# Kernel optimization log

Measured on AMD Instinct MI355X. Metric: run time of the kernel, lower is better.

Reference implementation:

```python
import jax, jax.numpy as jnp
import numpy as np

L_MAX = 119
D_MODEL = 128
N_HEADS = 4
HEAD_DIM = 32


def _rope_tables():
    # matches torch: inv_freq over arange(0,128,2)/128, t=arange(119), cast to bf16
    channel_range = jnp.arange(0, D_MODEL, 2, dtype=jnp.float32)
    inv_freq = 1.0 / (10000.0 ** (channel_range / D_MODEL))
    t = jnp.arange(L_MAX, dtype=jnp.float32)
    freqs = jnp.outer(t, inv_freq)  # (119, 64)
    return jnp.cos(freqs).astype(jnp.bfloat16), jnp.sin(freqs).astype(jnp.bfloat16)


def _apply_rotary(x, cos, sin):
    # x: (b, l, 128); half-rotation on the full model dim (pre head-split)
    l = x.shape[1]
    d = x.shape[-1] // 2
    x1, x2 = x[..., :d], x[..., d:]
    c, s = cos[:l], sin[:l]
    y1 = x1 * c + x2 * s
    y2 = x1 * (-s) + x2 * c
    return jnp.concatenate([y1, y2], axis=-1).astype(x.dtype)


def setup_inputs() -> dict:
    key = jax.random.key(0)
    k1, k2, k3, k4, k5 = jax.random.split(key, 5)
    b, l = 2048, L_MAX
    return {
        "x": jax.random.normal(k1, (b, l, D_MODEL), dtype=jnp.float32),
        "W_qkv": jax.random.normal(k2, (3 * D_MODEL, D_MODEL), dtype=jnp.float32) * 0.05,
        "b_qkv": jax.random.normal(k3, (3 * D_MODEL,), dtype=jnp.float32) * 0.02,
        "W_fc2": jax.random.normal(k4, (D_MODEL, D_MODEL), dtype=jnp.float32) * 0.05,
        "b_fc2": jax.random.normal(k5, (D_MODEL,), dtype=jnp.float32) * 0.02,
    }


def reference(x, W_qkv, b_qkv, W_fc2, b_fc2):
    b, l, _ = x.shape
    cos, sin = _rope_tables()

    qkv = x @ W_qkv.T + b_qkv  # (b, l, 384)
    q, k, v = jnp.split(qkv, 3, axis=-1)
    q = _apply_rotary(q, cos, sin)
    k = _apply_rotary(k, cos, sin)

    # faithful to source: view(b, l, 32, 4) then 'b l d h -> b h l d'
    def split_heads(t):
        return t.reshape(b, l, HEAD_DIM, N_HEADS).transpose(0, 3, 1, 2)  # (b, h, l, d)

    q, k, v = split_heads(q), split_heads(k), split_heads(v)

    scale = 1.0 / np.sqrt(HEAD_DIM)
    scores = jnp.einsum("bhld,bhmd->bhlm", q, k) * scale  # (b, h, l, l)
    causal = jnp.tril(jnp.ones((l, l), dtype=bool))
    scores = jnp.where(causal, scores, jnp.float32(-jnp.inf))
    attn = jax.nn.softmax(scores, axis=-1)
    y = jnp.einsum("bhlm,bhmd->bhld", attn, v)  # (b, h, l, d)

    # faithful to source: transpose(1,2) then view(b, l, 128) -> layout h*32+d
    y = y.transpose(0, 2, 1, 3).reshape(b, l, D_MODEL)
    y = y @ W_fc2.T + b_fc2
    return jax.nn.silu(y)
```

## Files before the change

kernel.cpp:

```cpp
#include <hip/hip_runtime.h>
#include <hip/hip_bf16.h>
#include <math.h>


#define L_SEQ 119
#define D_MODEL 128
#define SCALE 0.17677669529663687f
#define NEGINF -1e30f

typedef __bf16 bf16x8 __attribute__((ext_vector_type(8)));
typedef __bf16 bf16x2 __attribute__((ext_vector_type(2)));
typedef float f32x4 __attribute__((ext_vector_type(4)));
typedef float f32x16 __attribute__((ext_vector_type(16)));

__global__ void prep_kernel(const float* __restrict__ Wqkv,
                            const float* __restrict__ bqkv,
                            const float* __restrict__ Wfc2,
                            unsigned* __restrict__ tabu,
                            __bf16* __restrict__ Wb, float* __restrict__ bb2,
                            __bf16* __restrict__ Wf2b) {
  int i = blockIdx.x * 256 + threadIdx.x;
  {
    int j = i & 7, lane = (i >> 3) & 63, ks = (i >> 9) & 7, nt = i >> 12;
    int d = lane & 31;
    int h = nt / 3, qkv = nt % 3;
    int k = ks * 16 + (lane >> 5) * 8 + j;
    Wb[i] = (__bf16)Wqkv[(qkv * 128 + d * 4 + h) * 128 + k];
  }
  if (i < 384) {
    int nt2 = i >> 5, dd = i & 31;
    bb2[i] = bqkv[(nt2 % 3) * 128 + dd * 4 + (nt2 / 3)];
  }
  if (i < 16384) {
    int j = i & 7, lane = (i >> 3) & 63, kb = (i >> 9) & 3, nt = i >> 11;
    int n = nt * 16 + (lane & 15);
    int k = kb * 32 + (lane >> 4) * 8 + j;
    Wf2b[i] = (__bf16)Wfc2[n * 128 + k];
  }
  if (i < L_SEQ * 64) {
    int l = i >> 6, j = i & 63;
    float inv = 1.0f / powf(10000.0f, (float)(2 * j) / 128.0f);
    float f = (float)l * inv;
    union { bf16x2 v; unsigned u; } cs;
    cs.v[0] = (__bf16)cosf(f);
    cs.v[1] = (__bf16)sinf(f);
    tabu[i] = cs.u;
  }
}

__global__ __launch_bounds__(512) void fused_all(
    const float* __restrict__ x, const __bf16* __restrict__ Wb,
    const float* __restrict__ bb2, const unsigned* __restrict__ tabu,
    const __bf16* __restrict__ Wf2b, const float* __restrict__ bfc2,
    float* __restrict__ out) {
  __shared__ __align__(16) __bf16 qs[4 * 128 * 40];
  __shared__ __align__(16) __bf16 ksm[4 * 128 * 40];
  __shared__ __align__(16) __bf16 vT[4 * 32 * 128];
  __shared__ unsigned tabL[L_SEQ * 65];

  const int t = threadIdx.x, b = blockIdx.x;
  const int lane = t & 63, wv = t >> 6;
  const int ln31 = lane & 31, hi = lane >> 5;

  for (int i = t; i < L_SEQ * 64; i += 512)
    tabL[(i >> 6) * 65 + (i & 63)] = tabu[i];
  for (int i = t; i < 4 * 32 * 9; i += 512) {
    int hd = i / 9, cc = L_SEQ + i % 9, d = hd & 31;
    vT[hd * 128 + (cc ^ ((d & 7) << 3))] = (__bf16)0.0f;
  }
  __syncthreads();

  const int mt = wv & 3, g2 = wv >> 2;
  const int l_me = mt * 32 + ln31;
  const bool live = (l_me < L_SEQ);
  {
    int xr = live ? l_me : (L_SEQ - 1);
    const float* xrow = x + ((size_t)b * L_SEQ + xr) * 128;
    bf16x8 af[8];
#pragma unroll
    for (int ks = 0; ks < 8; ++ks) {
      float4 lo = *(const float4*)&xrow[ks * 16 + hi * 8];
      float4 hi4 = *(const float4*)&xrow[ks * 16 + hi * 8 + 4];
      bf16x8 v;
      v[0] = (__bf16)lo.x; v[1] = (__bf16)lo.y; v[2] = (__bf16)lo.z; v[3] = (__bf16)lo.w;
      v[4] = (__bf16)hi4.x; v[5] = (__bf16)hi4.y; v[6] = (__bf16)hi4.z; v[7] = (__bf16)hi4.w;
      af[ks] = v;
    }
#pragma unroll
    for (int r = 0; r < 3; ++r) {
      const int nt0 = g2 * 6 + 2 * r, nt1 = nt0 + 1;
      f32x16 a0 = {}, a1 = {};
#pragma unroll
      for (int ks = 0; ks < 8; ++ks) {
        bf16x8 wf0 = *(const bf16x8*)&Wb[(((nt0 * 8 + ks) * 64) + lane) * 8];
        bf16x8 wf1 = *(const bf16x8*)&Wb[(((nt1 * 8 + ks) * 64) + lane) * 8];
        a0 = __builtin_amdgcn_mfma_f32_32x32x16_bf16(wf0, af[ks], a0, 0, 0, 0);
        a1 = __builtin_amdgcn_mfma_f32_32x32x16_bf16(wf1, af[ks], a1, 0, 0, 0);
      }
#pragma unroll
      for (int e = 0; e < 2; ++e) {
        const int nt = e ? nt1 : nt0;
        const f32x16& A = e ? a1 : a0;
        const int h = nt / 3, qkv = nt % 3;
        if (qkv < 2) {
          __bf16* base = (qkv == 0) ? qs : ksm;
          if (live) {
#pragma unroll
            for (int rg = 0; rg < 8; ++rg) {
              const int c_lo = (rg & 3) + 8 * (rg >> 2);
              int d = c_lo + 4 * hi;
              union { bf16x2 v; unsigned u; } cs;
              cs.u = tabL[l_me * 65 + 4 * d + h];
              float c = (float)cs.v[0], s = (float)cs.v[1];
              float v1 = A[rg] + bb2[nt * 32 + d];
              float v2 = A[rg + 8] + bb2[nt * 32 + d + 16];
              if (qkv == 0) { v1 *= SCALE; v2 *= SCALE; }
              union { bf16x2 v; unsigned u; } pk;
              pk.v[0] = (__bf16)(v1 * c + v2 * s);
              pk.v[1] = (__bf16)(v2 * c - v1 * s);
              *(unsigned*)&base[(h * 128 + l_me) * 40 + 2 * d] = pk.u;
            }
          }
        } else {
          if (live) {
#pragma unroll
            for (int rg = 0; rg < 16; ++rg) {
              const int d = (rg & 3) + 8 * (rg >> 2) + 4 * hi;
              float val = A[rg] + bb2[nt * 32 + d];
              vT[(h * 32 + d) * 128 + (l_me ^ ((d & 7) << 3))] = (__bf16)val;
            }
          }
        }
      }
    }
  }
  __syncthreads();

  {
    const int h = wv >> 1;
#pragma unroll
    for (int ts = 0; ts < 2; ++ts) {
      const int qt = ts ? (3 - (wv & 1)) : (wv & 1);
      bf16x8 qf0 = *(const bf16x8*)&qs[(h * 128 + qt * 32 + ln31) * 40 + hi * 8];
      bf16x8 qf1 = *(const bf16x8*)&qs[(h * 128 + qt * 32 + ln31) * 40 + 16 + hi * 8];
      f32x16 s[4];
#pragma unroll
      for (int kt = 0; kt < 4; ++kt) {
        if (kt <= qt) {
          bf16x8 kf0 = *(const bf16x8*)&ksm[(h * 128 + kt * 32 + ln31) * 40 + hi * 8];
          bf16x8 kf1 = *(const bf16x8*)&ksm[(h * 128 + kt * 32 + ln31) * 40 + 16 + hi * 8];
          f32x16 z = {};
          z = __builtin_amdgcn_mfma_f32_32x32x16_bf16(kf0, qf0, z, 0, 0, 0);
          s[kt] = __builtin_amdgcn_mfma_f32_32x32x16_bf16(kf1, qf1, z, 0, 0, 0);
        }
      }
      {
#pragma unroll
        for (int rg = 0; rg < 16; ++rg) {
          const int c_lo = (rg & 3) + 8 * (rg >> 2);
#pragma unroll
          for (int kt = 0; kt < 4; ++kt) {
            if (kt == qt) {
              int crow = c_lo + 4 * hi;
              s[kt][rg] = (crow <= ln31) ? s[kt][rg] : NEGINF;
            }
          }
        }
      }
      float mx = NEGINF;
#pragma unroll
      for (int kt = 0; kt < 4; ++kt)
        if (kt <= qt)
#pragma unroll
          for (int rg = 0; rg < 16; ++rg) mx = fmaxf(mx, s[kt][rg]);
      mx = fmaxf(mx, __shfl_xor(mx, 32));
      float sum = 0.0f;
#pragma unroll
      for (int kt = 0; kt < 4; ++kt)
        if (kt <= qt)
#pragma unroll
          for (int rg = 0; rg < 16; ++rg) {
            s[kt][rg] = __expf(s[kt][rg] - mx);
            sum += s[kt][rg];
          }
      sum += __shfl_xor(sum, 32);
      float inv = 1.0f / sum;
      unsigned pk[4][8];
#pragma unroll
      for (int kt = 0; kt < 4; ++kt) {
        if (kt <= qt) {
#pragma unroll
          for (int p = 0; p < 8; ++p) {
            union { bf16x2 v; unsigned u; } w;
            w.v[0] = (__bf16)(s[kt][2 * p] * inv);
            w.v[1] = (__bf16)(s[kt][2 * p + 1] * inv);
            pk[kt][p] = w.u;
          }
        }
      }
      f32x16 o = {};
#pragma unroll
      for (int kt = 0; kt < 4; ++kt) {
        if (kt <= qt) {
#pragma unroll
          for (int m = 0; m < 2; ++m) {
            unsigned f0 = (unsigned)__shfl_xor((int)pk[kt][4 * m + 0], 32);
            unsigned f1 = (unsigned)__shfl_xor((int)pk[kt][4 * m + 1], 32);
            unsigned f2 = (unsigned)__shfl_xor((int)pk[kt][4 * m + 2], 32);
            unsigned f3 = (unsigned)__shfl_xor((int)pk[kt][4 * m + 3], 32);
            union { unsigned w[4]; bf16x8 v; } Aw;
            Aw.w[0] = hi ? f2 : pk[kt][4 * m + 0];
            Aw.w[1] = hi ? f3 : pk[kt][4 * m + 1];
            Aw.w[2] = hi ? pk[kt][4 * m + 2] : f0;
            Aw.w[3] = hi ? pk[kt][4 * m + 3] : f1;
            bf16x8 vf = *(const bf16x8*)&vT[(h * 32 + ln31) * 128 +
                ((kt * 32 + m * 16 + hi * 8) ^ ((ln31 & 7) << 3))];
            o = __builtin_amdgcn_mfma_f32_32x32x16_bf16(Aw.v, vf, o, 0, 0, 0);
          }
        }
      }
#pragma unroll
      for (int rg = 0; rg < 16; ++rg) {
        const int c_lo = (rg & 3) + 8 * (rg >> 2);
        int l = qt * 32 + c_lo + 4 * hi;
        if (l < L_SEQ)
          out[((size_t)b * L_SEQ + l) * 128 + h * 32 + ln31] = o[rg];
      }
    }
  }

  __syncthreads();
  {
    const int ln15 = lane & 15, kg = lane >> 4;
    int yr = wv * 16 + ln15;
    if (yr > L_SEQ - 1) yr = L_SEQ - 1;
    const float* yrow = out + ((size_t)b * L_SEQ + yr) * 128;
    bf16x8 af2[4];
#pragma unroll
    for (int kb = 0; kb < 4; ++kb) {
      float4 lo = *(const float4*)&yrow[kb * 32 + kg * 8];
      float4 hi4 = *(const float4*)&yrow[kb * 32 + kg * 8 + 4];
      bf16x8 v;
      v[0] = (__bf16)lo.x; v[1] = (__bf16)lo.y; v[2] = (__bf16)lo.z; v[3] = (__bf16)lo.w;
      v[4] = (__bf16)hi4.x; v[5] = (__bf16)hi4.y; v[6] = (__bf16)hi4.z; v[7] = (__bf16)hi4.w;
      af2[kb] = v;
    }
    float bc[8];
#pragma unroll
    for (int nt = 0; nt < 8; ++nt) bc[nt] = bfc2[nt * 16 + ln15];
    f32x4 acc2[8] = {};
#pragma unroll
    for (int nt = 0; nt < 8; ++nt)
#pragma unroll
      for (int kb = 0; kb < 4; ++kb)
        acc2[nt] = __builtin_amdgcn_mfma_f32_16x16x32_bf16(
            af2[kb], *(const bf16x8*)&Wf2b[(((nt * 4 + kb) * 64) + lane) * 8],
            acc2[nt], 0, 0, 0);
#pragma unroll
    for (int nt = 0; nt < 8; ++nt)
#pragma unroll
      for (int r = 0; r < 4; ++r) {
        int row = wv * 16 + kg * 4 + r, c = nt * 16 + ln15;
        if (row < L_SEQ) {
          float vv = acc2[nt][r] + bc[nt];
          out[((size_t)b * L_SEQ + row) * 128 + c] = vv / (1.0f + __expf(-vv));
        }
      }
  }
}

extern "C" void kernel_launch(void* const* d_in, const int* in_sizes, int n_in,
                              void* d_out, int out_size, void* d_ws,
                              size_t ws_size, hipStream_t stream) {
  const float* x = (const float*)d_in[0];
  const float* Wqkv = (const float*)d_in[1];
  const float* bqkv = (const float*)d_in[2];
  const float* Wfc2 = (const float*)d_in[3];
  const float* bfc2 = (const float*)d_in[4];
  float* out = (float*)d_out;

  char* ws = (char*)d_ws;
  unsigned* tabu = (unsigned*)ws;
  __bf16* Wb = (__bf16*)(ws + 30720);
  float* bb2 = (float*)(ws + 30720 + 98304);
  __bf16* Wf2b = (__bf16*)(ws + 30720 + 98304 + 1536);

  const int B = in_sizes[0] / (L_SEQ * D_MODEL);
  prep_kernel<<<192, 256, 0, stream>>>(Wqkv, bqkv, Wfc2, tabu, Wb, bb2, Wf2b);
  fused_all<<<B, 512, 0, stream>>>(x, Wb, bb2, tabu, Wf2b, bfc2, out);
}
```

Measured before the change: 217.6 us.

## Double block size to 1024 threads and split work across 16 waves

Launches 16 waves per block instead of 8. In the QKV stage each wave now computes one head's q/k/v tiles for one 32-row slab instead of six n-tiles. In attention each wave handles a single query tile instead of two. In FC2 each wave computes half of the output columns. The aim is to shorten each wave's serial chain and raise parallelism within the block, at the cost of higher register pressure under the 1024 launch bound and possible occupancy limits from LDS use per block.

```diff
diff --git a/kernel.cpp b/kernel.cpp
--- a/kernel.cpp
+++ b/kernel.cpp
@@ -48,7 +48,7 @@
   }
 }
 
-__global__ __launch_bounds__(512) void fused_all(
+__global__ __launch_bounds__(1024) void fused_all(
     const float* __restrict__ x, const __bf16* __restrict__ Wb,
     const float* __restrict__ bb2, const unsigned* __restrict__ tabu,
     const __bf16* __restrict__ Wf2b, const float* __restrict__ bfc2,
@@ -62,15 +62,15 @@
   const int lane = t & 63, wv = t >> 6;
   const int ln31 = lane & 31, hi = lane >> 5;
 
-  for (int i = t; i < L_SEQ * 64; i += 512)
+  for (int i = t; i < L_SEQ * 64; i += 1024)
     tabL[(i >> 6) * 65 + (i & 63)] = tabu[i];
-  for (int i = t; i < 4 * 32 * 9; i += 512) {
+  for (int i = t; i < 4 * 32 * 9; i += 1024) {
     int hd = i / 9, cc = L_SEQ + i % 9, d = hd & 31;
     vT[hd * 128 + (cc ^ ((d & 7) << 3))] = (__bf16)0.0f;
   }
   __syncthreads();
 
-  const int mt = wv & 3, g2 = wv >> 2;
+  const int mt = wv & 3, hd = wv >> 2;
   const int l_me = mt * 32 + ln31;
   const bool live = (l_me < L_SEQ);
   {
@@ -86,153 +86,148 @@
       v[4] = (__bf16)hi4.x; v[5] = (__bf16)hi4.y; v[6] = (__bf16)hi4.z; v[7] = (__bf16)hi4.w;
       af[ks] = v;
     }
-#pragma unroll
-    for (int r = 0; r < 3; ++r) {
-      const int nt0 = g2 * 6 + 2 * r, nt1 = nt0 + 1;
+    const int ntq = hd * 3;
+    {
       f32x16 a0 = {}, a1 = {};
 #pragma unroll
       for (int ks = 0; ks < 8; ++ks) {
-        bf16x8 wf0 = *(const bf16x8*)&Wb[(((nt0 * 8 + ks) * 64) + lane) * 8];
-        bf16x8 wf1 = *(const bf16x8*)&Wb[(((nt1 * 8 + ks) * 64) + lane) * 8];
+        bf16x8 wf0 = *(const bf16x8*)&Wb[(((ntq * 8 + ks) * 64) + lane) * 8];
+        bf16x8 wf1 = *(const bf16x8*)&Wb[((((ntq + 1) * 8 + ks) * 64) + lane) * 8];
         a0 = __builtin_amdgcn_mfma_f32_32x32x16_bf16(wf0, af[ks], a0, 0, 0, 0);
         a1 = __builtin_amdgcn_mfma_f32_32x32x16_bf16(wf1, af[ks], a1, 0, 0, 0);
       }
 #pragma unroll
       for (int e = 0; e < 2; ++e) {
-        const int nt = e ? nt1 : nt0;
         const f32x16& A = e ? a1 : a0;
-        const int h = nt / 3, qkv = nt % 3;
-        if (qkv < 2) {
-          __bf16* base = (qkv == 0) ? qs : ksm;
-          if (live) {
-#pragma unroll
-            for (int rg = 0; rg < 8; ++rg) {
-              const int c_lo = (rg & 3) + 8 * (rg >> 2);
-              int d = c_lo + 4 * hi;
-              union { bf16x2 v; unsigned u; } cs;
-              cs.u = tabL[l_me * 65 + 4 * d + h];
-              float c = (float)cs.v[0], s = (float)cs.v[1];
-              float v1 = A[rg] + bb2[nt * 32 + d];
-              float v2 = A[rg + 8] + bb2[nt * 32 + d + 16];
-              if (qkv == 0) { v1 *= SCALE; v2 *= SCALE; }
-              union { bf16x2 v; unsigned u; } pk;
-              pk.v[0] = (__bf16)(v1 * c + v2 * s);
-              pk.v[1] = (__bf16)(v2 * c - v1 * s);
-              *(unsigned*)&base[(h * 128 + l_me) * 40 + 2 * d] = pk.u;
-            }
+        const int nt = ntq + e;
+        __bf16* base = e ? ksm : qs;
+        if (live) {
+#pragma unroll
+          for (int rg = 0; rg < 8; ++rg) {
+            const int c_lo = (rg & 3) + 8 * (rg >> 2);
+            int d = c_lo + 4 * hi;
+            union { bf16x2 v; unsigned u; } cs;
+            cs.u = tabL[l_me * 65 + 4 * d + hd];
+            float c = (float)cs.v[0], s = (float)cs.v[1];
+            float v1 = A[rg] + bb2[nt * 32 + d];
+            float v2 = A[rg + 8] + bb2[nt * 32 + d + 16];
+            if (e == 0) { v1 *= SCALE; v2 *= SCALE; }
+            union { bf16x2 v; unsigned u; } pk;
+            pk.v[0] = (__bf16)(v1 * c + v2 * s);
+            pk.v[1] = (__bf16)(v2 * c - v1 * s);
+            *(unsigned*)&base[(hd * 128 + l_me) * 40 + 2 * d] = pk.u;
           }
-        } else {
-          if (live) {
-#pragma unroll
-            for (int rg = 0; rg < 16; ++rg) {
-              const int d = (rg & 3) + 8 * (rg >> 2) + 4 * hi;
-              float val = A[rg] + bb2[nt * 32 + d];
-              vT[(h * 32 + d) * 128 + (l_me ^ ((d & 7) << 3))] = (__bf16)val;
-            }
+        }
+      }
+    }
+    {
+      f32x16 a2 = {};
+#pragma unroll
+      for (int ks = 0; ks < 8; ++ks) {
+        bf16x8 wf2 = *(const bf16x8*)&Wb[((((ntq + 2) * 8 + ks) * 64) + lane) * 8];
+        a2 = __builtin_amdgcn_mfma_f32_32x32x16_bf16(wf2, af[ks], a2, 0, 0, 0);
+      }
+      if (live) {
+#pragma unroll
+        for (int rg = 0; rg < 16; ++rg) {
+          const int d = (rg & 3) + 8 * (rg >> 2) + 4 * hi;
+          float val = a2[rg] + bb2[(ntq + 2) * 32 + d];
+          vT[(hd * 32 + d) * 128 + (l_me ^ ((d & 7) << 3))] = (__bf16)val;
+        }
+      }
+    }
+  }
+  __syncthreads();
+
+  {
+    const int h = wv >> 2, qt = wv & 3;
+    bf16x8 qf0 = *(const bf16x8*)&qs[(h * 128 + qt * 32 + ln31) * 40 + hi * 8];
+    bf16x8 qf1 = *(const bf16x8*)&qs[(h * 128 + qt * 32 + ln31) * 40 + 16 + hi * 8];
+    f32x16 s[4];
+#pragma unroll
+    for (int kt = 0; kt < 4; ++kt) {
+      if (kt <= qt) {
+        bf16x8 kf0 = *(const bf16x8*)&ksm[(h * 128 + kt * 32 + ln31) * 40 + hi * 8];
+        bf16x8 kf1 = *(const bf16x8*)&ksm[(h * 128 + kt * 32 + ln31) * 40 + 16 + hi * 8];
+        f32x16 z = {};
+        z = __builtin_amdgcn_mfma_f32_32x32x16_bf16(kf0, qf0, z, 0, 0, 0);
+        s[kt] = __builtin_amdgcn_mfma_f32_32x32x16_bf16(kf1, qf1, z, 0, 0, 0);
+        if (kt == qt) {
+#pragma unroll
+          for (int rg = 0; rg < 16; ++rg) {
+            const int c_lo = (rg & 3) + 8 * (rg >> 2);
+            int crow = c_lo + 4 * hi;
+            s[kt][rg] = (crow <= ln31) ? s[kt][rg] : NEGINF;
           }
         }
       }
     }
-  }
+    float mx = NEGINF;
+#pragma unroll
+    for (int kt = 0; kt < 4; ++kt)
+      if (kt <= qt)
+#pragma unroll
+        for (int rg = 0; rg < 16; ++rg) mx = fmaxf(mx, s[kt][rg]);
+    mx = fmaxf(mx, __shfl_xor(mx, 32));
+    float sum = 0.0f;
+#pragma unroll
+    for (int kt = 0; kt < 4; ++kt)
+      if (kt <= qt)
+#pragma unroll
+        for (int rg = 0; rg < 16; ++rg) {
+          s[kt][rg] = __expf(s[kt][rg] - mx);
+          sum += s[kt][rg];
+        }
+    sum += __shfl_xor(sum, 32);
+    float inv = 1.0f / sum;
+    unsigned pk[4][8];
+#pragma unroll
+    for (int kt = 0; kt < 4; ++kt) {
+      if (kt <= qt) {
+#pragma unroll
+        for (int p = 0; p < 8; ++p) {
+          union { bf16x2 v; unsigned u; } w;
+          w.v[0] = (__bf16)(s[kt][2 * p] * inv);
+          w.v[1] = (__bf16)(s[kt][2 * p + 1] * inv);
+          pk[kt][p] = w.u;
+        }
+      }
+    }
+    f32x16 o = {};
+#pragma unroll
+    for (int kt = 0; kt < 4; ++kt) {
+      if (kt <= qt) {
+#pragma unroll
+        for (int m = 0; m < 2; ++m) {
+          unsigned f0 = (unsigned)__shfl_xor((int)pk[kt][4 * m + 0], 32);
+          unsigned f1 = (unsigned)__shfl_xor((int)pk[kt][4 * m + 1], 32);
+          unsigned f2 = (unsigned)__shfl_xor((int)pk[kt][4 * m + 2], 32);
+          unsigned f3 = (unsigned)__shfl_xor((int)pk[kt][4 * m + 3], 32);
+          union { unsigned w[4]; bf16x8 v; } Aw;
+          Aw.w[0] = hi ? f2 : pk[kt][4 * m + 0];
+          Aw.w[1] = hi ? f3 : pk[kt][4 * m + 1];
+          Aw.w[2] = hi ? pk[kt][4 * m + 2] : f0;
+          Aw.w[3] = hi ? pk[kt][4 * m + 3] : f1;
+          bf16x8 vf = *(const bf16x8*)&vT[(h * 32 + ln31) * 128 +
+              ((kt * 32 + m * 16 + hi * 8) ^ ((ln31 & 7) << 3))];
+          o = __builtin_amdgcn_mfma_f32_32x32x16_bf16(Aw.v, vf, o, 0, 0, 0);
+        }
+      }
+    }
+#pragma unroll
+    for (int rg = 0; rg < 16; ++rg) {
+      const int c_lo = (rg & 3) + 8 * (rg >> 2);
+      int l = qt * 32 + c_lo + 4 * hi;
+      if (l < L_SEQ)
+        out[((size_t)b * L_SEQ + l) * 128 + h * 32 + ln31] = o[rg];
+    }
+  }
+
   __syncthreads();
-
-  {
-    const int h = wv >> 1;
-#pragma unroll
-    for (int ts = 0; ts < 2; ++ts) {
-      const int qt = ts ? (3 - (wv & 1)) : (wv & 1);
-      bf16x8 qf0 = *(const bf16x8*)&qs[(h * 128 + qt * 32 + ln31) * 40 + hi * 8];
-      bf16x8 qf1 = *(const bf16x8*)&qs[(h * 128 + qt * 32 + ln31) * 40 + 16 + hi * 8];
-      f32x16 s[4];
-#pragma unroll
-      for (int kt = 0; kt < 4; ++kt) {
-        if (kt <= qt) {
-          bf16x8 kf0 = *(const bf16x8*)&ksm[(h * 128 + kt * 32 + ln31) * 40 + hi * 8];
-          bf16x8 kf1 = *(const bf16x8*)&ksm[(h * 128 + kt * 32 + ln31) * 40 + 16 + hi * 8];
-          f32x16 z = {};
-          z = __builtin_amdgcn_mfma_f32_32x32x16_bf16(kf0, qf0, z, 0, 0, 0);
-          s[kt] = __builtin_amdgcn_mfma_f32_32x32x16_bf16(kf1, qf1, z, 0, 0, 0);
-        }
-      }
-      {
-#pragma unroll
-        for (int rg = 0; rg < 16; ++rg) {
-          const int c_lo = (rg & 3) + 8 * (rg >> 2);
-#pragma unroll
-          for (int kt = 0; kt < 4; ++kt) {
-            if (kt == qt) {
-              int crow = c_lo + 4 * hi;
-              s[kt][rg] = (crow <= ln31) ? s[kt][rg] : NEGINF;
-            }
-          }
-        }
-      }
-      float mx = NEGINF;
-#pragma unroll
-      for (int kt = 0; kt < 4; ++kt)
-        if (kt <= qt)
-#pragma unroll
-          for (int rg = 0; rg < 16; ++rg) mx = fmaxf(mx, s[kt][rg]);
-      mx = fmaxf(mx, __shfl_xor(mx, 32));
-      float sum = 0.0f;
-#pragma unroll
-      for (int kt = 0; kt < 4; ++kt)
-        if (kt <= qt)
-#pragma unroll
-          for (int rg = 0; rg < 16; ++rg) {
-            s[kt][rg] = __expf(s[kt][rg] - mx);
-            sum += s[kt][rg];
-          }
-      sum += __shfl_xor(sum, 32);
-      float inv = 1.0f / sum;
-      unsigned pk[4][8];
-#pragma unroll
-      for (int kt = 0; kt < 4; ++kt) {
-        if (kt <= qt) {
-#pragma unroll
-          for (int p = 0; p < 8; ++p) {
-            union { bf16x2 v; unsigned u; } w;
-            w.v[0] = (__bf16)(s[kt][2 * p] * inv);
-            w.v[1] = (__bf16)(s[kt][2 * p + 1] * inv);
-            pk[kt][p] = w.u;
-          }
-        }
-      }
-      f32x16 o = {};
-#pragma unroll
-      for (int kt = 0; kt < 4; ++kt) {
-        if (kt <= qt) {
-#pragma unroll
-          for (int m = 0; m < 2; ++m) {
-            unsigned f0 = (unsigned)__shfl_xor((int)pk[kt][4 * m + 0], 32);
-            unsigned f1 = (unsigned)__shfl_xor((int)pk[kt][4 * m + 1], 32);
-            unsigned f2 = (unsigned)__shfl_xor((int)pk[kt][4 * m + 2], 32);
-            unsigned f3 = (unsigned)__shfl_xor((int)pk[kt][4 * m + 3], 32);
-            union { unsigned w[4]; bf16x8 v; } Aw;
-            Aw.w[0] = hi ? f2 : pk[kt][4 * m + 0];
-            Aw.w[1] = hi ? f3 : pk[kt][4 * m + 1];
-            Aw.w[2] = hi ? pk[kt][4 * m + 2] : f0;
-            Aw.w[3] = hi ? pk[kt][4 * m + 3] : f1;
-            bf16x8 vf = *(const bf16x8*)&vT[(h * 32 + ln31) * 128 +
-                ((kt * 32 + m * 16 + hi * 8) ^ ((ln31 & 7) << 3))];
-            o = __builtin_amdgcn_mfma_f32_32x32x16_bf16(Aw.v, vf, o, 0, 0, 0);
-          }
-        }
-      }
-#pragma unroll
-      for (int rg = 0; rg < 16; ++rg) {
-        const int c_lo = (rg & 3) + 8 * (rg >> 2);
-        int l = qt * 32 + c_lo + 4 * hi;
-        if (l < L_SEQ)
-          out[((size_t)b * L_SEQ + l) * 128 + h * 32 + ln31] = o[rg];
-      }
-    }
-  }
-
-  __syncthreads();
   {
     const int ln15 = lane & 15, kg = lane >> 4;
-    int yr = wv * 16 + ln15;
+    const int mrow = wv & 7, nh = wv >> 3;
+    int yr = mrow * 16 + ln15;
     if (yr > L_SEQ - 1) yr = L_SEQ - 1;
     const float* yrow = out + ((size_t)b * L_SEQ + yr) * 128;
     bf16x8 af2[4];
@@ -245,24 +240,25 @@
       v[4] = (__bf16)hi4.x; v[5] = (__bf16)hi4.y; v[6] = (__bf16)hi4.z; v[7] = (__bf16)hi4.w;
       af2[kb] = v;
     }
-    float bc[8];
-#pragma unroll
-    for (int nt = 0; nt < 8; ++nt) bc[nt] = bfc2[nt * 16 + ln15];
-    f32x4 acc2[8] = {};
-#pragma unroll
-    for (int nt = 0; nt < 8; ++nt)
+    float bc[4];
+#pragma unroll
+    for (int p = 0; p < 4; ++p) bc[p] = bfc2[(nh * 4 + p) * 16 + ln15];
+    f32x4 acc2[4] = {};
+#pragma unroll
+    for (int p = 0; p < 4; ++p)
 #pragma unroll
       for (int kb = 0; kb < 4; ++kb)
-        acc2[nt] = __builtin_amdgcn_mfma_f32_16x16x32_bf16(
-            af2[kb], *(const bf16x8*)&Wf2b[(((nt * 4 + kb) * 64) + lane) * 8],
-            acc2[nt], 0, 0, 0);
-#pragma unroll
-    for (int nt = 0; nt < 8; ++nt)
+        acc2[p] = __builtin_amdgcn_mfma_f32_16x16x32_bf16(
+            af2[kb],
+            *(const bf16x8*)&Wf2b[((((nh * 4 + p) * 4 + kb) * 64) + lane) * 8],
+            acc2[p], 0, 0, 0);
+#pragma unroll
+    for (int p = 0; p < 4; ++p)
 #pragma unroll
       for (int r = 0; r < 4; ++r) {
-        int row = wv * 16 + kg * 4 + r, c = nt * 16 + ln15;
+        int row = mrow * 16 + kg * 4 + r, c = (nh * 4 + p) * 16 + ln15;
         if (row < L_SEQ) {
-          float vv = acc2[nt][r] + bc[nt];
+          float vv = acc2[p][r] + bc[p];
           out[((size_t)b * L_SEQ + row) * 128 + c] = vv / (1.0f + __expf(-vv));
         }
       }
@@ -287,5 +283,5 @@
 
   const int B = in_sizes[0] / (L_SEQ * D_MODEL);
   prep_kernel<<<192, 256, 0, stream>>>(Wqkv, bqkv, Wfc2, tabu, Wb, bb2, Wf2b);
-  fused_all<<<B, 512, 0, stream>>>(x, Wb, bb2, tabu, Wf2b, bfc2, out);
+  fused_all<<<B, 1024, 0, stream>>>(x, Wb, bb2, tabu, Wf2b, bfc2, out);
 }
```

Result: slower. 224.6 us (+3.2%).
